# Optimization experiments

Hardware: AMD Instinct MI355X
Metric: run time of the kernel (lower is better)

## Reference

```python
import jax, jax.numpy as jnp
import numpy as np

N = 262144      # active voxels
K = 27          # kernel volume (3^3)
C_IN = 32
C_OUT = 64
BN_EPS = 1e-5


def setup_inputs() -> dict:
    key = jax.random.key(0)
    k1, k2, k3, k4 = jax.random.split(key, 4)
    x = jax.random.normal(k1, (N, C_IN), dtype=jnp.float32)
    # rulebook: for each output voxel, the input voxel feeding each of the K offsets
    idx = jax.random.randint(k2, (N, K), 0, N, dtype=jnp.int32)
    fan_in = K * C_IN
    W = jax.random.normal(k3, (K, C_IN, C_OUT), dtype=jnp.float32) / np.sqrt(fan_in)
    b = jax.random.normal(k4, (C_OUT,), dtype=jnp.float32) * 0.01
    gamma = jnp.ones((C_OUT,), dtype=jnp.float32)
    beta = jnp.zeros((C_OUT,), dtype=jnp.float32)
    return {"x": x, "W": W, "b": b, "gamma": gamma, "beta": beta, "idx": idx}


def reference(x, W, b, gamma, beta, idx):
    # gather -> GEMM (explicit_gemm rulebook conv): [N,K,C_in] x [K,C_in,C_out]
    gathered = x[idx]                                   # [N, K, C_in]
    y = jnp.einsum('nkc,kcd->nd', gathered, W) + b      # [N, C_out]
    # BatchNorm1d (training mode: biased batch statistics)
    mean = jnp.mean(y, axis=0)
    var = jnp.var(y, axis=0)
    y_hat = (y - mean) * jax.lax.rsqrt(var + BN_EPS)
    out = jax.nn.relu(y_hat * gamma + beta)
    return out
```

## Files before the change

kernel.cpp:

```cpp
#include <hip/hip_runtime.h>
#include <hip/hip_bf16.h>

#define NROWS 262144
#define KVOL  27
#define CIN   32
#define COUT  64
#define BN_EPS 1e-5f

using bf16x8 = __attribute__((ext_vector_type(8))) short;
using f32x4  = __attribute__((ext_vector_type(4))) float;

#define OFF_XB  0ull
#define OFF_WF  (16ull<<20)
#define OFF_ACC ((16ull<<20) + (128ull<<10))
#define OFF_SS  ((16ull<<20) + (128ull<<10) + 512ull)
#define OFF_Y   (17ull<<20)

__device__ __forceinline__ unsigned short f2bf(float f) {
    __hip_bfloat16 h = __float2bfloat16(f);
    return __builtin_bit_cast(unsigned short, h);
}

__global__ void k_cvt_x(const float4* __restrict__ x4, ushort4* __restrict__ xb4) {
    int i = blockIdx.x * 256 + threadIdx.x;
    float4 v = x4[i];
    ushort4 o;
    o.x = f2bf(v.x); o.y = f2bf(v.y); o.z = f2bf(v.z); o.w = f2bf(v.w);
    xb4[i] = o;
}

__global__ void k_repack_w(const float* __restrict__ W, __hip_bfloat16* __restrict__ wf,
                           float* __restrict__ gacc) {
    int kk = blockIdx.x;
    int tid = threadIdx.x;
    int t = tid >> 6, l = tid & 63;
    int c0 = (l >> 4) * 8;
    int co = t * 16 + (l & 15);
    __hip_bfloat16* dst = wf + ((size_t)(kk * 4 + t) * 64 + l) * 8;
    #pragma unroll
    for (int j = 0; j < 8; ++j) {
        float v = W[(size_t)(kk * CIN + c0 + j) * COUT + co];
        dst[j] = __float2bfloat16(v);
    }
    if (kk == 0 && tid < 128) gacc[tid] = 0.0f;
}

__global__ void __launch_bounds__(256)
k_gemm(const __hip_bfloat16* __restrict__ xb, const __hip_bfloat16* __restrict__ wf,
       const int* __restrict__ idx, __hip_bfloat16* __restrict__ y,
       float* __restrict__ gacc) {
    __shared__ float ssum[4][64];
    __shared__ float ssq[4][64];

    const int tid  = threadIdx.x;
    const int w    = tid >> 6;
    const int l    = tid & 63;
    const int lrow = l & 15;
    const int lk8  = l >> 4;
    const int rb   = blockIdx.x * 256 + w * 64;

    f32x4 acc[4][4] = {};
    const bf16x8* wf8 = (const bf16x8*)wf;

    for (int kk = 0; kk < KVOL; ++kk) {
        int id[4];
        #pragma unroll
        for (int m = 0; m < 4; ++m)
            id[m] = idx[(rb + m * 16 + lrow) * KVOL + kk];

        bf16x8 a[4];
        #pragma unroll
        for (int m = 0; m < 4; ++m)
            a[m] = *(const bf16x8*)(xb + (size_t)id[m] * CIN + lk8 * 8);

        bf16x8 bq[4];
        #pragma unroll
        for (int t = 0; t < 4; ++t)
            bq[t] = wf8[(kk * 4 + t) * 64 + l];

        #pragma unroll
        for (int m = 0; m < 4; ++m)
            #pragma unroll
            for (int t = 0; t < 4; ++t)
                acc[m][t] = __builtin_amdgcn_mfma_f32_16x16x32_bf16(a[m], bq[t], acc[m][t], 0, 0, 0);
    }

    float s[4] = {0, 0, 0, 0}, sq[4] = {0, 0, 0, 0};
    #pragma unroll
    for (int m = 0; m < 4; ++m) {
        #pragma unroll
        for (int r = 0; r < 4; ++r) {
            int row = rb + m * 16 + lk8 * 4 + r;
            #pragma unroll
            for (int t = 0; t < 4; ++t) {
                float v = acc[m][t][r];
                y[(size_t)row * COUT + t * 16 + lrow] = __float2bfloat16(v);
                s[t] += v;
                sq[t] += v * v;
            }
        }
    }
    #pragma unroll
    for (int t = 0; t < 4; ++t) {
        s[t]  += __shfl_xor(s[t], 16, 64);  s[t]  += __shfl_xor(s[t], 32, 64);
        sq[t] += __shfl_xor(sq[t], 16, 64); sq[t] += __shfl_xor(sq[t], 32, 64);
    }
    if (l < 16) {
        #pragma unroll
        for (int t = 0; t < 4; ++t) { ssum[w][t * 16 + l] = s[t]; ssq[w][t * 16 + l] = sq[t]; }
    }
    __syncthreads();
    if (tid < 64) {
        float ts = 0, tq = 0;
        #pragma unroll
        for (int ww = 0; ww < 4; ++ww) { ts += ssum[ww][tid]; tq += ssq[ww][tid]; }
        atomicAdd(&gacc[tid], ts);
        atomicAdd(&gacc[64 + tid], tq);
    }
}

__global__ void k_stats(const float* __restrict__ gacc, const float* __restrict__ gamma,
                        const float* __restrict__ beta, float* __restrict__ ss) {
    int c = threadIdx.x;
    float inv_n = 1.0f / (float)NROWS;
    float mean = gacc[c] * inv_n;
    float var  = gacc[64 + c] * inv_n - mean * mean;
    float rstd = rsqrtf(var + BN_EPS);
    float sc = gamma[c] * rstd;
    ss[c] = sc;
    ss[64 + c] = beta[c] - mean * sc;
}

__global__ void k_apply(const uint4* __restrict__ y8, const float* __restrict__ ss,
                        float* __restrict__ out) {
    const int nchunk = NROWS * COUT / 8;
    int i0 = blockIdx.x * blockDim.x + threadIdx.x;
    int c0 = (i0 * 8) & 63;
    float sc[8], sh[8];
    #pragma unroll
    for (int j = 0; j < 8; ++j) { sc[j] = ss[c0 + j]; sh[j] = ss[64 + c0 + j]; }
    for (int i = i0; i < nchunk; i += gridDim.x * blockDim.x) {
        uint4 v = y8[i];
        const unsigned short* p = (const unsigned short*)&v;
        float r[8];
        #pragma unroll
        for (int j = 0; j < 8; ++j) {
            float f = __uint_as_float((unsigned)p[j] << 16);
            r[j] = fmaxf(0.0f, f * sc[j] + sh[j]);
        }
        float4* o = (float4*)(out + (size_t)i * 8);
        o[0] = make_float4(r[0], r[1], r[2], r[3]);
        o[1] = make_float4(r[4], r[5], r[6], r[7]);
    }
}

extern "C" void kernel_launch(void* const* d_in, const int* in_sizes, int n_in,
                              void* d_out, int out_size, void* d_ws, size_t ws_size,
                              hipStream_t stream) {
    const float* x     = (const float*)d_in[0];
    const float* W     = (const float*)d_in[1];
    const float* gamma = (const float*)d_in[3];
    const float* beta  = (const float*)d_in[4];
    const int*   idx   = (const int*)d_in[5];

    char* ws = (char*)d_ws;
    __hip_bfloat16* xb   = (__hip_bfloat16*)(ws + OFF_XB);
    __hip_bfloat16* wf   = (__hip_bfloat16*)(ws + OFF_WF);
    float*          gacc = (float*)(ws + OFF_ACC);
    float*          ss   = (float*)(ws + OFF_SS);
    __hip_bfloat16* y    = (__hip_bfloat16*)(ws + OFF_Y);
    float*          out  = (float*)d_out;

    k_cvt_x<<<NROWS * CIN / (4 * 256), 256, 0, stream>>>((const float4*)x, (ushort4*)xb);
    k_repack_w<<<KVOL, 256, 0, stream>>>(W, wf, gacc);
    k_gemm<<<NROWS / 256, 256, 0, stream>>>(xb, wf, idx, y, gacc);
    k_stats<<<1, 64, 0, stream>>>(gacc, gamma, beta, ss);
    k_apply<<<2048, 256, 0, stream>>>((const uint4*)y, ss, out);
}
```

Measured before the change: 281.9 us.

## Fuse prep/stats kernels, stage rulebook in LDS, software-pipeline gathers in GEMM

Merges the x conversion and weight repack into one launch, and folds the BN stats computation into the apply kernel, cutting five launches to three. The GEMM now uses 128 rows per block (32 per wave) with more blocks and launch bounds requesting higher occupancy. Each block stages its idx slice in LDS with a coalesced copy, and gathers run two kernel offsets ahead of the MFMAs through a triple-buffered rotation. The risks are more register pressure from the in-flight buffers, and every apply block recomputing the per-channel scale and shift.

```diff
diff --git a/kernel.cpp b/kernel.cpp
--- a/kernel.cpp
+++ b/kernel.cpp
@@ -13,7 +13,6 @@
 #define OFF_XB  0ull
 #define OFF_WF  (16ull<<20)
 #define OFF_ACC ((16ull<<20) + (128ull<<10))
-#define OFF_SS  ((16ull<<20) + (128ull<<10) + 512ull)
 #define OFF_Y   (17ull<<20)
 
 __device__ __forceinline__ unsigned short f2bf(float f) {
@@ -21,34 +20,34 @@
     return __builtin_bit_cast(unsigned short, h);
 }
 
-__global__ void k_cvt_x(const float4* __restrict__ x4, ushort4* __restrict__ xb4) {
-    int i = blockIdx.x * 256 + threadIdx.x;
-    float4 v = x4[i];
-    ushort4 o;
-    o.x = f2bf(v.x); o.y = f2bf(v.y); o.z = f2bf(v.z); o.w = f2bf(v.w);
-    xb4[i] = o;
+__global__ void k_prep(const float4* __restrict__ x4, ushort4* __restrict__ xb4,
+                       const float* __restrict__ W, __hip_bfloat16* __restrict__ wf,
+                       float* __restrict__ gacc) {
+    int bid = blockIdx.x, tid = threadIdx.x;
+    if (bid < 8192) {
+        int i = bid * 256 + tid;
+        float4 v = x4[i];
+        ushort4 o;
+        o.x = f2bf(v.x); o.y = f2bf(v.y); o.z = f2bf(v.z); o.w = f2bf(v.w);
+        xb4[i] = o;
+    } else {
+        int kk = bid - 8192;
+        int t = tid >> 6, l = tid & 63;
+        int c0 = (l >> 4) * 8;
+        int co = t * 16 + (l & 15);
+        __hip_bfloat16* dst = wf + ((size_t)(kk * 4 + t) * 64 + l) * 8;
+        #pragma unroll
+        for (int j = 0; j < 8; ++j)
+            dst[j] = __float2bfloat16(W[(size_t)(kk * CIN + c0 + j) * COUT + co]);
+        if (kk == 0 && tid < 128) gacc[tid] = 0.0f;
+    }
 }
 
-__global__ void k_repack_w(const float* __restrict__ W, __hip_bfloat16* __restrict__ wf,
-                           float* __restrict__ gacc) {
-    int kk = blockIdx.x;
-    int tid = threadIdx.x;
-    int t = tid >> 6, l = tid & 63;
-    int c0 = (l >> 4) * 8;
-    int co = t * 16 + (l & 15);
-    __hip_bfloat16* dst = wf + ((size_t)(kk * 4 + t) * 64 + l) * 8;
-    #pragma unroll
-    for (int j = 0; j < 8; ++j) {
-        float v = W[(size_t)(kk * CIN + c0 + j) * COUT + co];
-        dst[j] = __float2bfloat16(v);
-    }
-    if (kk == 0 && tid < 128) gacc[tid] = 0.0f;
-}
-
-__global__ void __launch_bounds__(256)
+__global__ void __launch_bounds__(256, 5)
 k_gemm(const __hip_bfloat16* __restrict__ xb, const __hip_bfloat16* __restrict__ wf,
        const int* __restrict__ idx, __hip_bfloat16* __restrict__ y,
        float* __restrict__ gacc) {
+    __shared__ int s_idx[128 * KVOL];
     __shared__ float ssum[4][64];
     __shared__ float ssq[4][64];
 
@@ -57,37 +56,57 @@
     const int l    = tid & 63;
     const int lrow = l & 15;
     const int lk8  = l >> 4;
-    const int rb   = blockIdx.x * 256 + w * 64;
+    const int wrb  = w * 32;
+    const int rb   = blockIdx.x * 128 + wrb;
 
-    f32x4 acc[4][4] = {};
+    {
+        const int* src = idx + (size_t)blockIdx.x * 128 * KVOL;
+        for (int i = tid; i < 128 * KVOL; i += 256) s_idx[i] = src[i];
+    }
+    __syncthreads();
+
+    f32x4 acc[2][4] = {};
     const bf16x8* wf8 = (const bf16x8*)wf;
+    const int koff = lk8 * 8;
 
-    for (int kk = 0; kk < KVOL; ++kk) {
-        int id[4];
-        #pragma unroll
-        for (int m = 0; m < 4; ++m)
-            id[m] = idx[(rb + m * 16 + lrow) * KVOL + kk];
+#define LOADID(dst, KK) { dst##0 = s_idx[(wrb + lrow) * KVOL + (KK)]; \
+                          dst##1 = s_idx[(wrb + 16 + lrow) * KVOL + (KK)]; }
+#define GATHER(a, dst)  { a[0] = *(const bf16x8*)(xb + (unsigned)(dst##0 * CIN) + koff); \
+                          a[1] = *(const bf16x8*)(xb + (unsigned)(dst##1 * CIN) + koff); }
+#define LOADB(b, KK)    { _Pragma("unroll") for (int t = 0; t < 4; ++t) \
+                            b[t] = wf8[((KK) * 4 + t) * 64 + l]; }
+#define MFMA8(a, b)     { _Pragma("unroll") for (int m = 0; m < 2; ++m) \
+                          _Pragma("unroll") for (int t = 0; t < 4; ++t) \
+                            acc[m][t] = __builtin_amdgcn_mfma_f32_16x16x32_bf16(a[m], b[t], acc[m][t], 0, 0, 0); }
 
-        bf16x8 a[4];
-        #pragma unroll
-        for (int m = 0; m < 4; ++m)
-            a[m] = *(const bf16x8*)(xb + (size_t)id[m] * CIN + lk8 * 8);
+    bf16x8 aA[2], aB[2], aC[2];
+    int id_0, id_1;
 
-        bf16x8 bq[4];
-        #pragma unroll
-        for (int t = 0; t < 4; ++t)
-            bq[t] = wf8[(kk * 4 + t) * 64 + l];
+    LOADID(id_, 0); GATHER(aA, id_);
+    LOADID(id_, 1); GATHER(aB, id_);
 
-        #pragma unroll
-        for (int m = 0; m < 4; ++m)
-            #pragma unroll
-            for (int t = 0; t < 4; ++t)
-                acc[m][t] = __builtin_amdgcn_mfma_f32_16x16x32_bf16(a[m], bq[t], acc[m][t], 0, 0, 0);
+    #pragma unroll
+    for (int j = 0; j < 8; ++j) {
+        const int kk = j * 3;
+        bf16x8 b0[4], b1[4], b2[4];
+        LOADB(b0, kk);     LOADID(id_, kk + 2); GATHER(aC, id_); MFMA8(aA, b0);
+        LOADB(b1, kk + 1); LOADID(id_, kk + 3); GATHER(aA, id_); MFMA8(aB, b1);
+        LOADB(b2, kk + 2); LOADID(id_, kk + 4); GATHER(aB, id_); MFMA8(aC, b2);
     }
+    {
+        bf16x8 b0[4], b1[4], b2[4];
+        LOADB(b0, 24); LOADID(id_, 26); GATHER(aC, id_); MFMA8(aA, b0);
+        LOADB(b1, 25); MFMA8(aB, b1);
+        LOADB(b2, 26); MFMA8(aC, b2);
+    }
+#undef LOADID
+#undef GATHER
+#undef LOADB
+#undef MFMA8
 
     float s[4] = {0, 0, 0, 0}, sq[4] = {0, 0, 0, 0};
     #pragma unroll
-    for (int m = 0; m < 4; ++m) {
+    for (int m = 0; m < 2; ++m) {
         #pragma unroll
         for (int r = 0; r < 4; ++r) {
             int row = rb + m * 16 + lk8 * 4 + r;
@@ -119,26 +138,28 @@
     }
 }
 
-__global__ void k_stats(const float* __restrict__ gacc, const float* __restrict__ gamma,
-                        const float* __restrict__ beta, float* __restrict__ ss) {
-    int c = threadIdx.x;
-    float inv_n = 1.0f / (float)NROWS;
-    float mean = gacc[c] * inv_n;
-    float var  = gacc[64 + c] * inv_n - mean * mean;
-    float rstd = rsqrtf(var + BN_EPS);
-    float sc = gamma[c] * rstd;
-    ss[c] = sc;
-    ss[64 + c] = beta[c] - mean * sc;
-}
+__global__ void k_apply(const uint4* __restrict__ y8, const float* __restrict__ gacc,
+                        const float* __restrict__ gamma, const float* __restrict__ beta,
+                        float* __restrict__ out) {
+    __shared__ float s_sc[64], s_sh[64];
+    const int tid = threadIdx.x;
+    if (tid < 64) {
+        float inv_n = 1.0f / (float)NROWS;
+        float mean = gacc[tid] * inv_n;
+        float var  = gacc[64 + tid] * inv_n - mean * mean;
+        float rstd = rsqrtf(var + BN_EPS);
+        float sc = gamma[tid] * rstd;
+        s_sc[tid] = sc;
+        s_sh[tid] = beta[tid] - mean * sc;
+    }
+    __syncthreads();
 
-__global__ void k_apply(const uint4* __restrict__ y8, const float* __restrict__ ss,
-                        float* __restrict__ out) {
     const int nchunk = NROWS * COUT / 8;
-    int i0 = blockIdx.x * blockDim.x + threadIdx.x;
+    int i0 = blockIdx.x * blockDim.x + tid;
     int c0 = (i0 * 8) & 63;
     float sc[8], sh[8];
     #pragma unroll
-    for (int j = 0; j < 8; ++j) { sc[j] = ss[c0 + j]; sh[j] = ss[64 + c0 + j]; }
+    for (int j = 0; j < 8; ++j) { sc[j] = s_sc[c0 + j]; sh[j] = s_sh[c0 + j]; }
     for (int i = i0; i < nchunk; i += gridDim.x * blockDim.x) {
         uint4 v = y8[i];
         const unsigned short* p = (const unsigned short*)&v;
@@ -167,13 +188,10 @@
     __hip_bfloat16* xb   = (__hip_bfloat16*)(ws + OFF_XB);
     __hip_bfloat16* wf   = (__hip_bfloat16*)(ws + OFF_WF);
     float*          gacc = (float*)(ws + OFF_ACC);
-    float*          ss   = (float*)(ws + OFF_SS);
     __hip_bfloat16* y    = (__hip_bfloat16*)(ws + OFF_Y);
     float*          out  = (float*)d_out;
 
-    k_cvt_x<<<NROWS * CIN / (4 * 256), 256, 0, stream>>>((const float4*)x, (ushort4*)xb);
-    k_repack_w<<<KVOL, 256, 0, stream>>>(W, wf, gacc);
-    k_gemm<<<NROWS / 256, 256, 0, stream>>>(xb, wf, idx, y, gacc);
-    k_stats<<<1, 64, 0, stream>>>(gacc, gamma, beta, ss);
-    k_apply<<<2048, 256, 0, stream>>>((const uint4*)y, ss, out);
+    k_prep<<<8192 + KVOL, 256, 0, stream>>>((const float4*)x, (ushort4*)xb, W, wf, gacc);
+    k_gemm<<<NROWS / 128, 256, 0, stream>>>(xb, wf, idx, y, gacc);
+    k_apply<<<2048, 256, 0, stream>>>((const uint4*)y, gacc, gamma, beta, out);
 }
```

Result: faster. 237.1 us (-15.9%).
